# Kernel tuning notes

Hardware: AMD Instinct MI355X
Metric: run time of the kernel (lower is better)

## Reference

```python
import jax, jax.numpy as jnp
import numpy as np
from jax.scipy.linalg import solve_triangular

B, T, D, H, DK = 32, 256, 2048, 16, 64  # batch, chunk len, hidden, heads, head_dim


def setup_inputs() -> dict:
    key = jax.random.key(0)
    ks = jax.random.split(key, 7)
    s = 1.0 / np.sqrt(D)
    g = jnp.linspace(0.8, 0.999, H)
    return {
        'W_old': jax.random.normal(ks[0], (B, H, DK, DK), jnp.float32) * 0.02,
        'content': jax.random.normal(ks[1], (B, T, D), jnp.float32),
        'k_w': jax.random.normal(ks[2], (H * DK, D), jnp.float32) * s,
        'v_w': jax.random.normal(ks[3], (H * DK, D), jnp.float32) * s,
        'b_w': jax.random.normal(ks[4], (H, D), jnp.float32) * s,
        'b_b': jnp.zeros((H,), jnp.float32),
        'ts_w': jax.random.normal(ks[5], (H, D), jnp.float32) * 0.02,
        'ts_b': jnp.zeros((H,), jnp.float32),
        'hd_logits': jnp.log(g / (1.0 - g)).astype(jnp.float32),
    }


def _delta_write(W_old, content, k_w, v_w, b_w, b_b, ts_w, ts_b, hd_logits):
    # projections: (B,T,D) -> (B,H,T,d)
    k = (content @ k_w.T).reshape(B, T, H, DK).transpose(0, 2, 1, 3)
    v = (content @ v_w.T).reshape(B, T, H, DK).transpose(0, 2, 1, 3)
    k = k / jnp.clip(jnp.linalg.norm(k, axis=-1, keepdims=True), 1e-12)  # L2 normalize
    beta = jax.nn.sigmoid(content @ b_w.T + b_b).transpose(0, 2, 1)        # (B,H,T)
    gamma = jax.nn.sigmoid(hd_logits + content @ ts_w.T + ts_b).transpose(0, 2, 1)  # (B,H,T)

    # log-space prefix products of gamma
    log_gamma = jnp.log(jnp.clip(gamma, 1e-8))
    cum_log = jnp.cumsum(log_gamma, axis=-1)                               # (B,H,T)
    cum_log_im1 = jnp.pad(cum_log[..., :-1], ((0, 0), (0, 0), (1, 0)))     # G_{i-1}, G_0=1
    log_ratio = jnp.minimum(cum_log_im1[..., :, None] - cum_log[..., None, :], 0.0)
    ratio = jnp.exp(log_ratio)                                             # (B,H,T,T)
    G_im1 = jnp.exp(cum_log_im1)
    G_T = jnp.exp(cum_log[..., -1:])                                       # (B,H,1)

    # RHS: v_i - G_{i-1} W0 k_i
    W0k = jnp.einsum('bhvd,bhtd->bhtv', W_old, k)
    V_rhs = v - G_im1[..., None] * W0k

    # strictly-lower triangular system (I + A) V' = V_rhs
    KK = jnp.einsum('bhid,bhjd->bhij', k, k)
    A = beta[..., None, :] * ratio * KK
    tril = jnp.tril(jnp.ones((T, T), bool), k=-1)
    L = jnp.eye(T, dtype=A.dtype) + jnp.where(tril, A, 0.0)
    Vp = solve_triangular(L, V_rhs, lower=True, unit_diagonal=True)        # (B,H,T,d_v)

    decay_to_T = jnp.exp(cum_log[..., -1:] - cum_log)                      # (B,H,T)
    weighted = (beta * decay_to_T)[..., None] * Vp
    W_new = G_T[..., None] * W_old + jnp.einsum('bhtv,bhtd->bhvd', weighted, k)
    return W_new


def reference(W_old, content, k_w, v_w, b_w, b_b, ts_w, ts_b, hd_logits):
    return _delta_write(W_old, content, k_w, v_w, b_w, b_b, ts_w, ts_b, hd_logits)
```

## Files before the change

kernel.cpp:

```cpp
#include <hip/hip_runtime.h>
#include <hip/hip_bf16.h>
#include <math.h>

constexpr int B = 32, T = 256, D = 2048, H = 16, DK = 64;
constexpr size_t BHTD = (size_t)B * H * T * DK;
constexpr int NC8 = (B * T * D) / 8;
constexpr int NW8 = (H * DK * D) / 8;
constexpr int NB8 = (H * D) / 8;

typedef __attribute__((ext_vector_type(8))) short short8;
typedef __attribute__((ext_vector_type(4))) float f32x4;

#define MFMA16(a, b, c) __builtin_amdgcn_mfma_f32_16x16x32_bf16((a), (b), (c), 0, 0, 0)

__global__ __launch_bounds__(256) void cast_all(
    const float* __restrict__ content, const float* __restrict__ k_w,
    const float* __restrict__ v_w, const float* __restrict__ b_w,
    const float* __restrict__ ts_w, __hip_bfloat16* __restrict__ c_bf,
    __hip_bfloat16* __restrict__ w_bf) {
  const int total = NC8 + 2 * NW8 + 2 * NB8;
  int i = blockIdx.x * blockDim.x + threadIdx.x;
  const int stride = gridDim.x * blockDim.x;
  for (; i < total; i += stride) {
    const float* src;
    __hip_bfloat16* dst;
    int idx;
    if (i < NC8) { src = content; dst = c_bf; idx = i; }
    else if (i < NC8 + NW8) { src = k_w; dst = w_bf; idx = i - NC8; }
    else if (i < NC8 + 2 * NW8) {
      src = v_w; dst = w_bf + (size_t)1024 * D; idx = i - NC8 - NW8;
    } else if (i < NC8 + 2 * NW8 + NB8) {
      src = b_w; dst = w_bf + (size_t)2048 * D; idx = i - NC8 - 2 * NW8;
    } else {
      src = ts_w; dst = w_bf + (size_t)2064 * D; idx = i - NC8 - 2 * NW8 - NB8;
    }
    const float4 x = ((const float4*)src)[2 * idx];
    const float4 y = ((const float4*)src)[2 * idx + 1];
    __hip_bfloat16 tmp[8];
    tmp[0] = __float2bfloat16(x.x); tmp[1] = __float2bfloat16(x.y);
    tmp[2] = __float2bfloat16(x.z); tmp[3] = __float2bfloat16(x.w);
    tmp[4] = __float2bfloat16(y.x); tmp[5] = __float2bfloat16(y.y);
    tmp[6] = __float2bfloat16(y.z); tmp[7] = __float2bfloat16(y.w);
    *(uint4*)(dst + 8 * (size_t)idx) = *(const uint4*)tmp;
  }
}

__device__ __forceinline__ short8 ldsfrag128(const char* half_base, int row, int g) {
  return *(const short8*)(half_base + row * 128 + ((g ^ (row & 7)) << 4));
}

#define GBAR()                                   \
  do {                                           \
    asm volatile("" ::: "memory");               \
    __builtin_amdgcn_sched_barrier(0);           \
    __builtin_amdgcn_s_barrier();                \
    __builtin_amdgcn_sched_barrier(0);           \
  } while (0)

__global__ __launch_bounds__(512, 2) void gemm256(
    const __hip_bfloat16* __restrict__ A, const __hip_bfloat16* __restrict__ Wc,
    float* __restrict__ outk) {
  extern __shared__ char smem[];
  const int tid = threadIdx.x;
  const int w = tid >> 6, l = tid & 63;
  const int wm = w >> 2, wn = w & 3;
  const int fr = l & 15, fq = l >> 4;
  const int x = blockIdx.x & 7, q = (blockIdx.x >> 3) & 3, nt = blockIdx.x >> 5;
  const int mt = x * 4 + q;
  const int m0 = mt * 256, n0 = nt * 256;
  const int lrow = l >> 3;
  const int lg = ((l & 7) ^ lrow) * 8;

  auto stage = [&](const __hip_bfloat16* gbase, char* lds_half) {
#pragma unroll
    for (int r = 0; r < 2; ++r) {
      __builtin_amdgcn_global_load_lds(
          (const __attribute__((address_space(1))) void*)(
              gbase + (size_t)(r * 64 + w * 8 + lrow) * D + lg),
          (__attribute__((address_space(3))) void*)(lds_half + r * 8192 + w * 1024),
          16, 0, 0);
    }
  };
  auto issue = [&](int h) {
    if (h >= 128) return;
    const int tau = h >> 2, s = h & 3;
    const int k0 = tau * 64;
    char* base = smem + ((s < 2) ? 65536 : 0) + ((tau & 1) * 2 + (s & 1)) * 16384;
    const __hip_bfloat16* g = (s < 2)
        ? (Wc + (size_t)(n0 + (s & 1) * 128) * D + k0)
        : (A + (size_t)(m0 + (s & 1) * 128) * D + k0);
    stage(g, base);
  };

  for (int h = 0; h < 7; ++h) issue(h);
  asm volatile("s_waitcnt vmcnt(6)" ::: "memory");
  GBAR();

  f32x4 acc[8][4] = {};
  for (int tau = 0; tau < 32; ++tau) {
    const char* Ah = smem + ((tau & 1) * 2 + wm) * 16384;
    const char* Bh = smem + 65536 + ((tau & 1) * 2 + (wn >> 1)) * 16384;
    const int br0 = (wn & 1) * 64;
    short8 b0[4], b1[4], aA[2], aB[2], aC[2], aD[2];

#pragma unroll
    for (int j = 0; j < 4; ++j) {
      b0[j] = ldsfrag128(Bh, br0 + j * 16 + fr, fq);
      b1[j] = ldsfrag128(Bh, br0 + j * 16 + fr, 4 + fq);
    }
#pragma unroll
    for (int kk = 0; kk < 2; ++kk) {
      aA[kk] = ldsfrag128(Ah, 0 * 16 + fr, kk * 4 + fq);
      aB[kk] = ldsfrag128(Ah, 1 * 16 + fr, kk * 4 + fq);
    }
    issue(4 * tau + 7);
    GBAR();
    asm volatile("s_waitcnt lgkmcnt(0)" ::: "memory");
    __builtin_amdgcn_sched_barrier(0);
    __builtin_amdgcn_s_setprio(1);
#pragma unroll
    for (int j = 0; j < 4; ++j) {
      acc[0][j] = MFMA16(aA[0], b0[j], acc[0][j]);
      acc[0][j] = MFMA16(aA[1], b1[j], acc[0][j]);
      acc[1][j] = MFMA16(aB[0], b0[j], acc[1][j]);
      acc[1][j] = MFMA16(aB[1], b1[j], acc[1][j]);
    }
    __builtin_amdgcn_s_setprio(0);
    GBAR();

#pragma unroll
    for (int kk = 0; kk < 2; ++kk) {
      aA[kk] = ldsfrag128(Ah, 2 * 16 + fr, kk * 4 + fq);
      aB[kk] = ldsfrag128(Ah, 3 * 16 + fr, kk * 4 + fq);
    }
    issue(4 * tau + 8);
    GBAR();
    asm volatile("s_waitcnt lgkmcnt(0)" ::: "memory");
    __builtin_amdgcn_sched_barrier(0);
    __builtin_amdgcn_s_setprio(1);
#pragma unroll
    for (int j = 0; j < 4; ++j) {
      acc[2][j] = MFMA16(aA[0], b0[j], acc[2][j]);
      acc[2][j] = MFMA16(aA[1], b1[j], acc[2][j]);
      acc[3][j] = MFMA16(aB[0], b0[j], acc[3][j]);
      acc[3][j] = MFMA16(aB[1], b1[j], acc[3][j]);
    }
    __builtin_amdgcn_s_setprio(0);
    GBAR();

#pragma unroll
    for (int kk = 0; kk < 2; ++kk) {
      aA[kk] = ldsfrag128(Ah, 4 * 16 + fr, kk * 4 + fq);
      aB[kk] = ldsfrag128(Ah, 5 * 16 + fr, kk * 4 + fq);
      aC[kk] = ldsfrag128(Ah, 6 * 16 + fr, kk * 4 + fq);
      aD[kk] = ldsfrag128(Ah, 7 * 16 + fr, kk * 4 + fq);
    }
    issue(4 * tau + 9);
    GBAR();
    asm volatile("s_waitcnt lgkmcnt(0)" ::: "memory");
    __builtin_amdgcn_sched_barrier(0);
    __builtin_amdgcn_s_setprio(1);
#pragma unroll
    for (int j = 0; j < 4; ++j) {
      acc[4][j] = MFMA16(aA[0], b0[j], acc[4][j]);
      acc[4][j] = MFMA16(aA[1], b1[j], acc[4][j]);
      acc[5][j] = MFMA16(aB[0], b0[j], acc[5][j]);
      acc[5][j] = MFMA16(aB[1], b1[j], acc[5][j]);
    }
    __builtin_amdgcn_s_setprio(0);
    GBAR();

    issue(4 * tau + 10);
    GBAR();
    __builtin_amdgcn_s_setprio(1);
#pragma unroll
    for (int j = 0; j < 4; ++j) {
      acc[6][j] = MFMA16(aC[0], b0[j], acc[6][j]);
      acc[6][j] = MFMA16(aC[1], b1[j], acc[6][j]);
      acc[7][j] = MFMA16(aD[0], b0[j], acc[7][j]);
      acc[7][j] = MFMA16(aD[1], b1[j], acc[7][j]);
    }
    __builtin_amdgcn_s_setprio(0);
    if (tau < 30) asm volatile("s_waitcnt vmcnt(6)" ::: "memory");
    else asm volatile("s_waitcnt vmcnt(0)" ::: "memory");
    GBAR();
  }

#pragma unroll
  for (int i = 0; i < 8; ++i) {
    const int mbase = m0 + wm * 128 + i * 16 + fq * 4;
#pragma unroll
    for (int j = 0; j < 4; ++j) {
      const int n = n0 + wn * 64 + j * 16 + fr;
      const int h = (n >> 6) & 15, dk = n & 63;
      float* dst = outk + (size_t)(n >> 10) * BHTD;
#pragma unroll
      for (int r = 0; r < 4; ++r) {
        const int mm = mbase + r;
        const int b = mm >> 8, t = mm & 255;
        dst[(((size_t)b * H + h) * T + t) * DK + dk] = acc[i][j][r];
      }
    }
  }
}

__global__ __launch_bounds__(256) void bg_gemm(
    const __hip_bfloat16* __restrict__ A, const __hip_bfloat16* __restrict__ Wbg,
    const float* __restrict__ b_b, const float* __restrict__ ts_b,
    const float* __restrict__ hd, float* __restrict__ beta_out,
    float* __restrict__ gamma_out) {
  __shared__ float part[2][64][8];
  const int tid = threadIdx.x, w = tid >> 6, l = tid & 63;
  const int fr = l & 15, fq = l >> 4;
  const int wr = w & 1, wk = w >> 1;
  const int m0 = blockIdx.x * 32 + wr * 16;
  f32x4 acc0 = {0.f, 0.f, 0.f, 0.f}, acc1 = {0.f, 0.f, 0.f, 0.f};
  const __hip_bfloat16* ar = A + (size_t)(m0 + fr) * D + fq * 8 + wk * 1024;
  const __hip_bfloat16* br = Wbg + (size_t)fr * D + fq * 8 + wk * 1024;
  const __hip_bfloat16* gr = Wbg + (size_t)(16 + fr) * D + fq * 8 + wk * 1024;
#pragma unroll 4
  for (int k0 = 0; k0 < 1024; k0 += 32) {
    short8 af = *(const short8*)(ar + k0);
    short8 bfb = *(const short8*)(br + k0);
    short8 bfg = *(const short8*)(gr + k0);
    acc0 = MFMA16(af, bfb, acc0);
    acc1 = MFMA16(af, bfg, acc1);
  }
  if (wk == 1) {
#pragma unroll
    for (int r = 0; r < 4; ++r) {
      part[wr][l][r] = acc0[r];
      part[wr][l][4 + r] = acc1[r];
    }
  }
  __syncthreads();
  if (wk == 0) {
#pragma unroll
    for (int r = 0; r < 4; ++r) {
      acc0[r] += part[wr][l][r];
      acc1[r] += part[wr][l][4 + r];
    }
    const float bb = b_b[fr], bg = ts_b[fr] + hd[fr];
#pragma unroll
    for (int r = 0; r < 4; ++r) {
      const int mm = m0 + fq * 4 + r;
      const int b = mm >> 8, t = mm & 255;
      const size_t oo = ((size_t)b * H + fr) * T + t;
      beta_out[oo] = 1.f / (1.f + __expf(-(acc0[r] + bb)));
      gamma_out[oo] = 1.f / (1.f + __expf(-(acc1[r] + bg)));
    }
  }
}

__device__ __forceinline__ float rdlane(float x, int j) {
  return __int_as_float(__builtin_amdgcn_readlane(__float_as_int(x), j));
}
__device__ __forceinline__ int bofs(int row, int col) {
  return row * 128 + ((((col >> 3) ^ (row & 7))) << 4) + ((col & 7) << 1);
}
__device__ __forceinline__ short8 ldsfrag(const __hip_bfloat16* base, int row, int g0) {
  return *(const short8*)((const char*)base + row * 128 + (((g0 ^ (row & 7))) << 4));
}

#define SBAR()                                           \
  do {                                                   \
    __builtin_amdgcn_sched_barrier(0);                   \
    asm volatile("s_waitcnt lgkmcnt(0)" ::: "memory");   \
    __builtin_amdgcn_s_barrier();                        \
    __builtin_amdgcn_sched_barrier(0);                   \
  } while (0)

__global__ __launch_bounds__(256, 2) void solve_write(
    const float* __restrict__ kg, const float* __restrict__ vg,
    const float* __restrict__ betag, const float* __restrict__ gammag,
    const float* __restrict__ Wold, float* __restrict__ Wnew) {
  __shared__ __hip_bfloat16 kCb[64 * 64];
  __shared__ __hip_bfloat16 kTb[64 * 64];
  __shared__ __hip_bfloat16 Mb[64 * 64];
  __shared__ __hip_bfloat16 Ub[64 * 64];
  __shared__ float Ss[64][68];
  __shared__ float Uu[64][68];
  __shared__ float s_beta[256], s_cl[256];
  __shared__ float wpart[4];

  const int tid = threadIdx.x;
  const int bh = blockIdx.x;
  const size_t base = (size_t)bh * T * DK;
  const int lane = tid & 63, w = tid >> 6;
  const int fr = lane & 15, fq = lane >> 4;
  const int sr = tid >> 2, sp = tid & 3;

  s_beta[tid] = betag[(size_t)bh * T + tid];
  float xls = __logf(fmaxf(gammag[(size_t)bh * T + tid], 1e-8f));
#pragma unroll
  for (int d = 1; d < 64; d <<= 1) {
    float y = __shfl_up(xls, d, 64);
    if (lane >= d) xls += y;
  }
  if (lane == 63) wpart[w] = xls;
  __syncthreads();
  {
    float off = 0.f;
    if (w > 0) off += wpart[0];
    if (w > 1) off += wpart[1];
    if (w > 2) off += wpart[2];
    s_cl[tid] = xls + off;
  }
  f32x4 mreg[4];
  {
    const float* Wo = Wold + (size_t)bh * DK * DK;
#pragma unroll
    for (int j = 0; j < 4; ++j)
#pragma unroll
      for (int r = 0; r < 4; ++r)
        mreg[j][r] = Wo[(size_t)(16 * w + fq * 4 + r) * DK + 16 * j + fr];
  }
  const float4* kgp = (const float4*)(kg + base + (size_t)sr * DK) + sp * 4;
  const float* vbase = vg + base + (size_t)(16 * w + fq * 4) * DK + fr;
  float4 kx0 = kgp[0], kx1 = kgp[1], kx2 = kgp[2], kx3 = kgp[3];
  float vv[16];
#pragma unroll
  for (int j = 0; j < 4; ++j)
#pragma unroll
    for (int r = 0; r < 4; ++r)
      vv[4 * j + r] = vbase[(size_t)r * DK + 16 * j];
  SBAR();

  for (int c = 0; c < 4; ++c) {
    const int c0 = c * 64;
    const float oc = (c == 0) ? 0.f : s_cl[c0 - 1];
    const float on = s_cl[c0 + 63];

    {
#pragma unroll
      for (int j = 0; j < 4; ++j)
#pragma unroll
        for (int rr = 0; rr < 4; ++rr) {
          __hip_bfloat16 h = __float2bfloat16(mreg[j][rr]);
          *(short*)((char*)Mb + bofs(16 * w + fq * 4 + rr, 16 * j + fr)) = *(short*)&h;
        }
      const float4 x0 = kx0, x1 = kx1, x2 = kx2, x3 = kx3;
      float nrm = x0.x * x0.x + x0.y * x0.y + x0.z * x0.z + x0.w * x0.w +
                  x1.x * x1.x + x1.y * x1.y + x1.z * x1.z + x1.w * x1.w +
                  x2.x * x2.x + x2.y * x2.y + x2.z * x2.z + x2.w * x2.w +
                  x3.x * x3.x + x3.y * x3.y + x3.z * x3.z + x3.w * x3.w;
      nrm += __shfl_xor(nrm, 1, 64);
      nrm += __shfl_xor(nrm, 2, 64);
      const float rn = 1.f / fmaxf(sqrtf(nrm), 1e-12f);
      float kvf[16] = {x0.x * rn, x0.y * rn, x0.z * rn, x0.w * rn,
                       x1.x * rn, x1.y * rn, x1.z * rn, x1.w * rn,
                       x2.x * rn, x2.y * rn, x2.z * rn, x2.w * rn,
                       x3.x * rn, x3.y * rn, x3.z * rn, x3.w * rn};
      short kb[16];
#pragma unroll
      for (int u = 0; u < 16; ++u) {
        __hip_bfloat16 h = __float2bfloat16(kvf[u]);
        kb[u] = *(short*)&h;
      }
      *(short8*)((char*)kCb + sr * 128 + (((2 * sp) ^ (sr & 7)) << 4)) = *(short8*)&kb[0];
      *(short8*)((char*)kCb + sr * 128 + (((2 * sp + 1) ^ (sr & 7)) << 4)) = *(short8*)&kb[8];
#pragma unroll
      for (int u = 0; u < 16; ++u)
        *(short*)((char*)kTb + bofs(16 * sp + u, sr)) = kb[u];
    }
    SBAR();

    {
      const short8 af0 = ldsfrag(kCb, 16 * w + fr, fq);
      const short8 af1 = ldsfrag(kCb, 16 * w + fr, 4 + fq);
      const f32x4 zero = {0.f, 0.f, 0.f, 0.f};
#pragma unroll
      for (int j = 0; j < 4; ++j) {
        short8 b0 = ldsfrag(kCb, 16 * j + fr, fq);
        short8 b1 = ldsfrag(kCb, 16 * j + fr, 4 + fq);
        f32x4 s4 = MFMA16(af0, b0, zero);
        s4 = MFMA16(af1, b1, s4);
#pragma unroll
        for (int r = 0; r < 4; ++r) Ss[16 * w + fq * 4 + r][16 * j + fr] = s4[r];
      }
      float eci[4];
#pragma unroll
      for (int r = 0; r < 4; ++r) {
        const int gi = c0 + 16 * w + fq * 4 + r;
        eci[r] = __expf((gi == 0) ? 0.f : s_cl[gi - 1] - oc);
      }
#pragma unroll
      for (int j = 0; j < 4; ++j) {
        short8 m0 = ldsfrag(Mb, 16 * j + fr, fq);
        short8 m1 = ldsfrag(Mb, 16 * j + fr, 4 + fq);
        f32x4 u4 = MFMA16(af0, m0, zero);
        u4 = MFMA16(af1, m1, u4);
#pragma unroll
        for (int r = 0; r < 4; ++r) {
          const int t = 16 * w + fq * 4 + r;
          Uu[t][16 * j + fr] = vv[4 * j + r] - eci[r] * u4[r];
        }
      }
      if (c < 3) {
        const float4* kn = kgp + (size_t)(c + 1) * 1024;
        kx0 = kn[0]; kx1 = kn[1]; kx2 = kn[2]; kx3 = kn[3];
        const float* vn = vbase + (size_t)(c0 + 64) * DK;
#pragma unroll
        for (int j = 0; j < 4; ++j)
#pragma unroll
          for (int r = 0; r < 4; ++r)
            vv[4 * j + r] = vn[(size_t)r * DK + 16 * j];
      }
    }
    SBAR();

    {
      const int gi = c0 + lane;
      const int v0 = w * 16;
      float rhs[16];
#pragma unroll
      for (int u = 0; u < 4; ++u)
        *(float4*)&rhs[4 * u] = *(const float4*)&Uu[lane][v0 + 4 * u];
      const float ci = (gi == 0) ? 0.f : s_cl[gi - 1] - oc;
      const float ecl = __expf(ci);
      const float wgt = s_beta[gi] * __expf(-(s_cl[gi] - oc));
      for (int j = 0; j < 63; ++j) {
        const float wj = rdlane(wgt, j);
        const float sv = Ss[j][lane];
        const float co = (lane > j) ? ecl * wj * sv : 0.f;
#pragma unroll
        for (int u = 0; u < 16; ++u) rhs[u] -= co * rdlane(rhs[u], j);
      }
      const float ul = wgt * __expf(on - oc);
#pragma unroll
      for (int u = 0; u < 16; ++u) {
        __hip_bfloat16 h = __float2bfloat16(ul * rhs[u]);
        *(short*)((char*)Ub + bofs(v0 + u, lane)) = *(short*)&h;
      }
    }
    SBAR();

    {
      const float rc = __expf(on - oc);
      const short8 a0 = ldsfrag(Ub, 16 * w + fr, fq);
      const short8 a1 = ldsfrag(Ub, 16 * w + fr, 4 + fq);
#pragma unroll
      for (int j = 0; j < 4; ++j) {
        short8 b0 = ldsfrag(kTb, 16 * j + fr, fq);
        short8 b1 = ldsfrag(kTb, 16 * j + fr, 4 + fq);
        f32x4 c4;
#pragma unroll
        for (int r = 0; r < 4; ++r) c4[r] = rc * mreg[j][r];
        c4 = MFMA16(a0, b0, c4);
        c4 = MFMA16(a1, b1, c4);
        mreg[j] = c4;
      }
    }
    SBAR();
  }
  {
    float* op = Wnew + (size_t)bh * DK * DK;
#pragma unroll
    for (int j = 0; j < 4; ++j)
#pragma unroll
      for (int r = 0; r < 4; ++r)
        op[(size_t)(16 * w + fq * 4 + r) * DK + 16 * j + fr] = mreg[j][r];
  }
}

extern "C" void kernel_launch(void* const* d_in, const int* in_sizes, int n_in,
                              void* d_out, int out_size, void* d_ws, size_t ws_size,
                              hipStream_t stream) {
  const float* W_old = (const float*)d_in[0];
  const float* content = (const float*)d_in[1];
  const float* k_w = (const float*)d_in[2];
  const float* v_w = (const float*)d_in[3];
  const float* b_w = (const float*)d_in[4];
  const float* b_b = (const float*)d_in[5];
  const float* ts_w = (const float*)d_in[6];
  const float* ts_b = (const float*)d_in[7];
  const float* hd = (const float*)d_in[8];
  float* out = (float*)d_out;

  float* ws_k = (float*)d_ws;
  float* ws_v = ws_k + BHTD;
  float* ws_beta = ws_v + BHTD;
  float* ws_gamma = ws_beta + (size_t)B * H * T;
  __hip_bfloat16* c_bf = (__hip_bfloat16*)(ws_gamma + (size_t)B * H * T);
  __hip_bfloat16* w_bf = c_bf + (size_t)B * T * D;

  static int attr_done = 0;
  if (!attr_done) {
    hipFuncSetAttribute(reinterpret_cast<const void*>(gemm256),
                        hipFuncAttributeMaxDynamicSharedMemorySize, 131072);
    attr_done = 1;
  }

  cast_all<<<2048, 256, 0, stream>>>(content, k_w, v_w, b_w, ts_w, c_bf, w_bf);
  gemm256<<<dim3(256), dim3(512), 131072, stream>>>(c_bf, w_bf, ws_k);
  bg_gemm<<<dim3(256), dim3(256), 0, stream>>>(c_bf, w_bf + (size_t)2048 * D,
                                               b_b, ts_b, hd, ws_beta, ws_gamma);
  solve_write<<<dim3(B * H), 256, 0, stream>>>(ws_k, ws_v, ws_beta, ws_gamma,
                                               W_old, out);
}
```

Measured before the change: 274.5 us.

## Split solve_write over value columns and widen bg_gemm split-K

The solve kernel now launches two blocks per (batch, head), each owning 32 of the 64 value columns. Each block keeps half the W state and does half of the triangular-solve RHS work. Shared memory is aliased across phases and launch bounds raise occupancy to 4 blocks per CU. bg_gemm moves from a 2-way to a 4-way K split with 16-row tiles and twice as many blocks. The cost is duplicated k normalisation, KK computation and the cumsum in both halves, plus an extra barrier per chunk.

New measurement: 274.6 us. No clear change (+0.0%).

```diff
diff --git a/kernel.cpp b/kernel.cpp
--- a/kernel.cpp
+++ b/kernel.cpp
@@ -209,37 +209,38 @@
     const float* __restrict__ b_b, const float* __restrict__ ts_b,
     const float* __restrict__ hd, float* __restrict__ beta_out,
     float* __restrict__ gamma_out) {
-  __shared__ float part[2][64][8];
+  __shared__ float part[3][64][8];
   const int tid = threadIdx.x, w = tid >> 6, l = tid & 63;
   const int fr = l & 15, fq = l >> 4;
-  const int wr = w & 1, wk = w >> 1;
-  const int m0 = blockIdx.x * 32 + wr * 16;
+  const int m0 = blockIdx.x * 16;
   f32x4 acc0 = {0.f, 0.f, 0.f, 0.f}, acc1 = {0.f, 0.f, 0.f, 0.f};
-  const __hip_bfloat16* ar = A + (size_t)(m0 + fr) * D + fq * 8 + wk * 1024;
-  const __hip_bfloat16* br = Wbg + (size_t)fr * D + fq * 8 + wk * 1024;
-  const __hip_bfloat16* gr = Wbg + (size_t)(16 + fr) * D + fq * 8 + wk * 1024;
+  const __hip_bfloat16* ar = A + (size_t)(m0 + fr) * D + fq * 8 + w * 512;
+  const __hip_bfloat16* br = Wbg + (size_t)fr * D + fq * 8 + w * 512;
+  const __hip_bfloat16* gr = Wbg + (size_t)(16 + fr) * D + fq * 8 + w * 512;
 #pragma unroll 4
-  for (int k0 = 0; k0 < 1024; k0 += 32) {
+  for (int k0 = 0; k0 < 512; k0 += 32) {
     short8 af = *(const short8*)(ar + k0);
     short8 bfb = *(const short8*)(br + k0);
     short8 bfg = *(const short8*)(gr + k0);
     acc0 = MFMA16(af, bfb, acc0);
     acc1 = MFMA16(af, bfg, acc1);
   }
-  if (wk == 1) {
+  if (w > 0) {
 #pragma unroll
     for (int r = 0; r < 4; ++r) {
-      part[wr][l][r] = acc0[r];
-      part[wr][l][4 + r] = acc1[r];
+      part[w - 1][l][r] = acc0[r];
+      part[w - 1][l][4 + r] = acc1[r];
     }
   }
   __syncthreads();
-  if (wk == 0) {
-#pragma unroll
-    for (int r = 0; r < 4; ++r) {
-      acc0[r] += part[wr][l][r];
-      acc1[r] += part[wr][l][4 + r];
-    }
+  if (w == 0) {
+#pragma unroll
+    for (int p = 0; p < 3; ++p)
+#pragma unroll
+      for (int r = 0; r < 4; ++r) {
+        acc0[r] += part[p][l][r];
+        acc1[r] += part[p][l][4 + r];
+      }
     const float bb = b_b[fr], bg = ts_b[fr] + hd[fr];
 #pragma unroll
     for (int r = 0; r < 4; ++r) {
@@ -270,24 +271,28 @@
     __builtin_amdgcn_sched_barrier(0);                   \
   } while (0)
 
-__global__ __launch_bounds__(256, 2) void solve_write(
+__global__ __launch_bounds__(256, 4) void solve_write(
     const float* __restrict__ kg, const float* __restrict__ vg,
     const float* __restrict__ betag, const float* __restrict__ gammag,
     const float* __restrict__ Wold, float* __restrict__ Wnew) {
-  __shared__ __hip_bfloat16 kCb[64 * 64];
   __shared__ __hip_bfloat16 kTb[64 * 64];
-  __shared__ __hip_bfloat16 Mb[64 * 64];
-  __shared__ __hip_bfloat16 Ub[64 * 64];
+  __shared__ char regA[9216];
+  __shared__ char regB[4096];
   __shared__ float Ss[64][68];
-  __shared__ float Uu[64][68];
   __shared__ float s_beta[256], s_cl[256];
-  __shared__ float wpart[4];
+
+  __hip_bfloat16* kCb = (__hip_bfloat16*)regA;
+  float (*Uu)[36] = (float(*)[36])regA;
+  __hip_bfloat16* Mb = (__hip_bfloat16*)regB;
+  __hip_bfloat16* Ub = (__hip_bfloat16*)regB;
+  float* wpart = (float*)Ss;
 
   const int tid = threadIdx.x;
-  const int bh = blockIdx.x;
+  const int bh = blockIdx.x & 511, vs = blockIdx.x >> 9;
   const size_t base = (size_t)bh * T * DK;
   const int lane = tid & 63, w = tid >> 6;
   const int fr = lane & 15, fq = lane >> 4;
+  const int wv = w & 1, wd = w >> 1;
   const int sr = tid >> 2, sp = tid & 3;
 
   s_beta[tid] = betag[(size_t)bh * T + tid];
@@ -306,24 +311,24 @@
     if (w > 2) off += wpart[2];
     s_cl[tid] = xls + off;
   }
-  f32x4 mreg[4];
+  f32x4 mreg[2];
   {
-    const float* Wo = Wold + (size_t)bh * DK * DK;
-#pragma unroll
-    for (int j = 0; j < 4; ++j)
+    const float* Wo = Wold + (size_t)bh * DK * DK + (size_t)(32 * vs) * DK;
+#pragma unroll
+    for (int jj = 0; jj < 2; ++jj)
 #pragma unroll
       for (int r = 0; r < 4; ++r)
-        mreg[j][r] = Wo[(size_t)(16 * w + fq * 4 + r) * DK + 16 * j + fr];
+        mreg[jj][r] = Wo[(size_t)(16 * wv + fq * 4 + r) * DK + 16 * (2 * wd + jj) + fr];
   }
   const float4* kgp = (const float4*)(kg + base + (size_t)sr * DK) + sp * 4;
-  const float* vbase = vg + base + (size_t)(16 * w + fq * 4) * DK + fr;
+  const float* vbase = vg + base + (size_t)(16 * w + fq * 4) * DK + 32 * vs + fr;
   float4 kx0 = kgp[0], kx1 = kgp[1], kx2 = kgp[2], kx3 = kgp[3];
-  float vv[16];
-#pragma unroll
-  for (int j = 0; j < 4; ++j)
+  float vv[8];
+#pragma unroll
+  for (int jj = 0; jj < 2; ++jj)
 #pragma unroll
     for (int r = 0; r < 4; ++r)
-      vv[4 * j + r] = vbase[(size_t)r * DK + 16 * j];
+      vv[4 * jj + r] = vbase[(size_t)r * DK + 16 * jj];
   SBAR();
 
   for (int c = 0; c < 4; ++c) {
@@ -333,11 +338,12 @@
 
     {
 #pragma unroll
-      for (int j = 0; j < 4; ++j)
+      for (int jj = 0; jj < 2; ++jj)
 #pragma unroll
         for (int rr = 0; rr < 4; ++rr) {
-          __hip_bfloat16 h = __float2bfloat16(mreg[j][rr]);
-          *(short*)((char*)Mb + bofs(16 * w + fq * 4 + rr, 16 * j + fr)) = *(short*)&h;
+          __hip_bfloat16 h = __float2bfloat16(mreg[jj][rr]);
+          *(short*)((char*)Mb + bofs(16 * wv + fq * 4 + rr, 16 * (2 * wd + jj) + fr)) =
+              *(short*)&h;
         }
       const float4 x0 = kx0, x1 = kx1, x2 = kx2, x3 = kx3;
       float nrm = x0.x * x0.x + x0.y * x0.y + x0.z * x0.z + x0.w * x0.w +
@@ -365,9 +371,9 @@
     }
     SBAR();
 
+    const short8 af0 = ldsfrag(kCb, 16 * w + fr, fq);
+    const short8 af1 = ldsfrag(kCb, 16 * w + fr, 4 + fq);
     {
-      const short8 af0 = ldsfrag(kCb, 16 * w + fr, fq);
-      const short8 af1 = ldsfrag(kCb, 16 * w + fr, 4 + fq);
       const f32x4 zero = {0.f, 0.f, 0.f, 0.f};
 #pragma unroll
       for (int j = 0; j < 4; ++j) {
@@ -378,6 +384,11 @@
 #pragma unroll
         for (int r = 0; r < 4; ++r) Ss[16 * w + fq * 4 + r][16 * j + fr] = s4[r];
       }
+    }
+    SBAR();
+
+    {
+      const f32x4 zero = {0.f, 0.f, 0.f, 0.f};
       float eci[4];
 #pragma unroll
       for (int r = 0; r < 4; ++r) {
@@ -385,37 +396,35 @@
         eci[r] = __expf((gi == 0) ? 0.f : s_cl[gi - 1] - oc);
       }
 #pragma unroll
-      for (int j = 0; j < 4; ++j) {
-        short8 m0 = ldsfrag(Mb, 16 * j + fr, fq);
-        short8 m1 = ldsfrag(Mb, 16 * j + fr, 4 + fq);
+      for (int jj = 0; jj < 2; ++jj) {
+        short8 m0 = ldsfrag(Mb, 16 * jj + fr, fq);
+        short8 m1 = ldsfrag(Mb, 16 * jj + fr, 4 + fq);
         f32x4 u4 = MFMA16(af0, m0, zero);
         u4 = MFMA16(af1, m1, u4);
 #pragma unroll
         for (int r = 0; r < 4; ++r) {
           const int t = 16 * w + fq * 4 + r;
-          Uu[t][16 * j + fr] = vv[4 * j + r] - eci[r] * u4[r];
+          Uu[t][16 * jj + fr] = vv[4 * jj + r] - eci[r] * u4[r];
         }
       }
       if (c < 3) {
         const float4* kn = kgp + (size_t)(c + 1) * 1024;
         kx0 = kn[0]; kx1 = kn[1]; kx2 = kn[2]; kx3 = kn[3];
-        const float* vn = vbase + (size_t)(c0 + 64) * DK;
-#pragma unroll
-        for (int j = 0; j < 4; ++j)
+#pragma unroll
+        for (int jj = 0; jj < 2; ++jj)
 #pragma unroll
           for (int r = 0; r < 4; ++r)
-            vv[4 * j + r] = vn[(size_t)r * DK + 16 * j];
+            vv[4 * jj + r] = vbase[(size_t)(c0 + 64 + r) * DK + 16 * jj];
       }
     }
     SBAR();
 
     {
       const int gi = c0 + lane;
-      const int v0 = w * 16;
-      float rhs[16];
-#pragma unroll
-      for (int u = 0; u < 4; ++u)
-        *(float4*)&rhs[4 * u] = *(const float4*)&Uu[lane][v0 + 4 * u];
+      const int v0 = 8 * w;
+      float rhs[8];
+      *(float4*)&rhs[0] = *(const float4*)&Uu[lane][v0];
+      *(float4*)&rhs[4] = *(const float4*)&Uu[lane][v0 + 4];
       const float ci = (gi == 0) ? 0.f : s_cl[gi - 1] - oc;
       const float ecl = __expf(ci);
       const float wgt = s_beta[gi] * __expf(-(s_cl[gi] - oc));
@@ -424,11 +433,11 @@
         const float sv = Ss[j][lane];
         const float co = (lane > j) ? ecl * wj * sv : 0.f;
 #pragma unroll
-        for (int u = 0; u < 16; ++u) rhs[u] -= co * rdlane(rhs[u], j);
+        for (int u = 0; u < 8; ++u) rhs[u] -= co * rdlane(rhs[u], j);
       }
       const float ul = wgt * __expf(on - oc);
 #pragma unroll
-      for (int u = 0; u < 16; ++u) {
+      for (int u = 0; u < 8; ++u) {
         __hip_bfloat16 h = __float2bfloat16(ul * rhs[u]);
         *(short*)((char*)Ub + bofs(v0 + u, lane)) = *(short*)&h;
       }
@@ -437,18 +446,18 @@
 
     {
       const float rc = __expf(on - oc);
-      const short8 a0 = ldsfrag(Ub, 16 * w + fr, fq);
-      const short8 a1 = ldsfrag(Ub, 16 * w + fr, 4 + fq);
-#pragma unroll
-      for (int j = 0; j < 4; ++j) {
-        short8 b0 = ldsfrag(kTb, 16 * j + fr, fq);
-        short8 b1 = ldsfrag(kTb, 16 * j + fr, 4 + fq);
+      const short8 a0 = ldsfrag(Ub, 16 * wv + fr, fq);
+      const short8 a1 = ldsfrag(Ub, 16 * wv + fr, 4 + fq);
+#pragma unroll
+      for (int jj = 0; jj < 2; ++jj) {
+        short8 b0 = ldsfrag(kTb, 16 * (2 * wd + jj) + fr, fq);
+        short8 b1 = ldsfrag(kTb, 16 * (2 * wd + jj) + fr, 4 + fq);
         f32x4 c4;
 #pragma unroll
-        for (int r = 0; r < 4; ++r) c4[r] = rc * mreg[j][r];
+        for (int r = 0; r < 4; ++r) c4[r] = rc * mreg[jj][r];
         c4 = MFMA16(a0, b0, c4);
         c4 = MFMA16(a1, b1, c4);
-        mreg[j] = c4;
+        mreg[jj] = c4;
       }
     }
     SBAR();
@@ -456,10 +465,11 @@
   {
     float* op = Wnew + (size_t)bh * DK * DK;
 #pragma unroll
-    for (int j = 0; j < 4; ++j)
+    for (int jj = 0; jj < 2; ++jj)
 #pragma unroll
       for (int r = 0; r < 4; ++r)
-        op[(size_t)(16 * w + fq * 4 + r) * DK + 16 * j + fr] = mreg[j][r];
+        op[(size_t)(32 * vs + 16 * wv + fq * 4 + r) * DK + 16 * (2 * wd + jj) + fr] =
+            mreg[jj][r];
   }
 }
 
@@ -493,8 +503,8 @@
 
   cast_all<<<2048, 256, 0, stream>>>(content, k_w, v_w, b_w, ts_w, c_bf, w_bf);
   gemm256<<<dim3(256), dim3(512), 131072, stream>>>(c_bf, w_bf, ws_k);
-  bg_gemm<<<dim3(256), dim3(256), 0, stream>>>(c_bf, w_bf + (size_t)2048 * D,
-                                               b_b, ts_b, hd, ws_beta, ws_gamma);
-  solve_write<<<dim3(B * H), 256, 0, stream>>>(ws_k, ws_v, ws_beta, ws_gamma,
-                                               W_old, out);
-}
+  bg_gemm<<<dim3(512), 256, 0, stream>>>(c_bf, w_bf + (size_t)2048 * D,
+                                         b_b, ts_b, hd, ws_beta, ws_gamma);
+  solve_write<<<dim3(2 * B * H), 256, 0, stream>>>(ws_k, ws_v, ws_beta, ws_gamma,
+                                                   W_old, out);
+}
```
